# Kernel optimization log

Measured on AMD Instinct MI355X. Metric: run time of the kernel, lower is better.

Reference implementation:

```python
import jax, jax.numpy as jnp
import numpy as np

IN_F, N_ASS, OUT_F = 256, 4096, 256
P_CONNECT = 0.05
BATCH = 128


def _build_graph(in_f, n_ass, out_f, p, seed=0):
    """Replicates Random_RNN.random_graph_init edge structure (numpy, deterministic)."""
    rng = np.random.default_rng(seed)
    ass0 = in_f
    out0 = in_f + n_ass
    total = out0 + out_f
    # input -> associative edges, each input guaranteed >=1 outgoing edge
    m1 = rng.random((in_f, n_ass)) < p
    for i in np.where(~m1.any(axis=1))[0]:
        m1[i, rng.integers(n_ass)] = True
    in_src, in_dst = np.nonzero(m1)
    in_dst = in_dst + ass0
    # associative -> (associative | output) edges, each assoc >=1 outgoing edge
    m2 = rng.random((n_ass, n_ass + out_f)) < p
    for i in np.where(~m2.any(axis=1))[0]:
        m2[i, rng.integers(n_ass + out_f)] = True
    a_src, a_dst = np.nonzero(m2)
    a_src = a_src + ass0
    a_dst = a_dst + ass0
    # every output neuron guaranteed >=1 incoming edge from an associative neuron
    no_in = np.where(~m2[:, n_ass:].any(axis=0))[0]
    if no_in.size:
        a_src = np.concatenate([a_src, ass0 + rng.integers(0, n_ass, size=no_in.size)])
        a_dst = np.concatenate([a_dst, out0 + no_in])
    return (in_src.astype(np.int32), in_dst.astype(np.int32),
            a_src.astype(np.int32), a_dst.astype(np.int32), total)


def setup_inputs() -> dict:
    key = jax.random.key(0)
    k_x, k_wi, k_wa = jax.random.split(key, 3)
    in_src, in_dst, ass_src, ass_dst, total = _build_graph(IN_F, N_ASS, OUT_F, P_CONNECT)
    x = jax.random.normal(k_x, (BATCH, IN_F), dtype=jnp.float32)
    input_weights = jax.random.normal(k_wi, (in_src.shape[0],), dtype=jnp.float32) * 0.05
    associative_weights = jax.random.normal(k_wa, (ass_src.shape[0],), dtype=jnp.float32) * 0.05
    return {
        "x": x,
        "input_weights": input_weights,
        "associative_weights": associative_weights,
        "in_src": jnp.asarray(in_src),
        "in_dst": jnp.asarray(in_dst),
        "ass_src": jnp.asarray(ass_src),
        "ass_dst": jnp.asarray(ass_dst),
        "total_neurons": int(total),
        "out_features": OUT_F,
    }


def reference(x, input_weights, associative_weights, in_src, in_dst, ass_src, ass_dst,
              total_neurons, out_features):
    # Hop 1: input neurons emit x along their edges to associative neurons.
    # msg1: [E_in, B] = gather of input activations scaled by per-edge weight.
    msg1 = x.T[in_src] * input_weights[:, None]
    acc = jax.ops.segment_sum(msg1, in_dst, num_segments=total_neurons)  # [N, B]
    # Hop 2: associative neurons propagate along their edges (to assoc + output).
    msg2 = acc[ass_src] * associative_weights[:, None]  # [E_ass, B]
    acc2 = jax.ops.segment_sum(msg2, ass_dst, num_segments=total_neurons)  # [N, B]
    # Read activations of output neurons (last out_features node indices).
    return acc2[total_neurons - out_features:].T  # [B, out_features]
```

## Files before the change

kernel.cpp:

```cpp
#include <hip/hip_runtime.h>

#define IN_F   256
#define N_ASS  4096
#define OUT_F  256
#define BATCH  128
#define ASS0   256
#define OUT0   4352
#define SPLITK2 32

#define OFF_W2T (1024 * 1024)
#define OFF_P1  (2 * 1024 * 1024)
#define OFF_P2  (4 * 1024 * 1024)

__global__ __launch_bounds__(256) void zero_kernel(float4* __restrict__ w) {
    const int i = blockIdx.x * 256 + threadIdx.x;
    w[i] = make_float4(0.f, 0.f, 0.f, 0.f);
}

__global__ __launch_bounds__(256) void scatter_kernel(
        const int* __restrict__ src1, const int* __restrict__ dst1,
        const float* __restrict__ w1, int E1,
        const int* __restrict__ src2, const int* __restrict__ dst2,
        const float* __restrict__ w2, int E2,
        float* __restrict__ W1T, float* __restrict__ W2T) {
    const int e = blockIdx.x * 256 + threadIdx.x;
    if (e < E1) {
        W1T[src1[e] * N_ASS + (dst1[e] - ASS0)] = w1[e];
    } else if (e - E1 < E2) {
        const int i = e - E1;
        const int d = dst2[i];
        if (d >= OUT0)
            W2T[(src2[i] - ASS0) * OUT_F + (d - OUT0)] = w2[i];
    }
}

template<int N_, bool DUAL_A>
__global__ __launch_bounds__(256) void gemm64(const float* __restrict__ A, int lda,
                                              const float* __restrict__ B,
                                              float* __restrict__ P) {
    __shared__ __align__(16) float As[64][68];
    __shared__ __align__(16) float Bs[64][68];

    const int tid = threadIdx.x;
    const int m0 = blockIdx.x * 64;
    const int n0 = blockIdx.y * 64;
    const int z  = blockIdx.z;
    const int kBeg = z * 128;

    float4 areg[4], breg[4];
    #pragma unroll
    for (int r = 0; r < 4; ++r) {
        const int j = tid + r * 256;
        const float* ap = A + (size_t)(m0 + (j >> 4)) * lda + kBeg + (j & 15) * 4;
        areg[r] = *(const float4*)ap;
        if constexpr (DUAL_A) {
            const float4 a2 = *(const float4*)(ap + (size_t)BATCH * lda);
            areg[r].x += a2.x; areg[r].y += a2.y; areg[r].z += a2.z; areg[r].w += a2.w;
        }
        breg[r] = *(const float4*)(B + (size_t)(kBeg + (j >> 4)) * N_ + n0 + (j & 15) * 4);
    }

    const int ty4 = (tid >> 4) * 4;
    const int tx4 = (tid & 15) * 4;
    float c[4][4] = {};

    #pragma unroll
    for (int it = 0; it < 2; ++it) {
        if (it) __syncthreads();
        #pragma unroll
        for (int r = 0; r < 4; ++r) {
            const int j = tid + r * 256;
            *(float4*)&As[j >> 4][(j & 15) * 4] = areg[r];
            *(float4*)&Bs[j >> 4][(j & 15) * 4] = breg[r];
        }
        __syncthreads();
        if (it == 0) {
            const int k0 = kBeg + 64;
            #pragma unroll
            for (int r = 0; r < 4; ++r) {
                const int j = tid + r * 256;
                const float* ap = A + (size_t)(m0 + (j >> 4)) * lda + k0 + (j & 15) * 4;
                areg[r] = *(const float4*)ap;
                if constexpr (DUAL_A) {
                    const float4 a2 = *(const float4*)(ap + (size_t)BATCH * lda);
                    areg[r].x += a2.x; areg[r].y += a2.y; areg[r].z += a2.z; areg[r].w += a2.w;
                }
                breg[r] = *(const float4*)(B + (size_t)(k0 + (j >> 4)) * N_ + n0 + (j & 15) * 4);
            }
        }
        #pragma unroll
        for (int kk = 0; kk < 64; kk += 4) {
            float4 ar[4];
            #pragma unroll
            for (int i = 0; i < 4; ++i) ar[i] = *(const float4*)&As[ty4 + i][kk];
            #pragma unroll
            for (int u = 0; u < 4; ++u) {
                const float4 b = *(const float4*)&Bs[kk + u][tx4];
                #pragma unroll
                for (int i = 0; i < 4; ++i) {
                    const float a = ((const float*)&ar[i])[u];
                    c[i][0] = fmaf(a, b.x, c[i][0]);
                    c[i][1] = fmaf(a, b.y, c[i][1]);
                    c[i][2] = fmaf(a, b.z, c[i][2]);
                    c[i][3] = fmaf(a, b.w, c[i][3]);
                }
            }
        }
    }

    float* Pz = P + (size_t)z * (BATCH * N_);
    #pragma unroll
    for (int i = 0; i < 4; ++i)
        *(float4*)&Pz[(size_t)(m0 + ty4 + i) * N_ + n0 + tx4] =
            make_float4(c[i][0], c[i][1], c[i][2], c[i][3]);
}

__global__ __launch_bounds__(128) void reduce_kernel(const float4* __restrict__ P4,
                                                     float4* __restrict__ out4) {
    const int g = blockIdx.x * 128 + threadIdx.x;
    float4 s = make_float4(0.f, 0.f, 0.f, 0.f);
    #pragma unroll
    for (int z = 0; z < SPLITK2; ++z) {
        const float4 p = P4[(size_t)z * 8192 + g];
        s.x += p.x; s.y += p.y; s.z += p.z; s.w += p.w;
    }
    out4[g] = s;
}

extern "C" void kernel_launch(void* const* d_in, const int* in_sizes, int n_in,
                              void* d_out, int out_size, void* d_ws, size_t ws_size,
                              hipStream_t stream) {
    const float* x      = (const float*)d_in[0];
    const float* w_in   = (const float*)d_in[1];
    const float* w_ass  = (const float*)d_in[2];
    const int*   in_src = (const int*)d_in[3];
    const int*   in_dst = (const int*)d_in[4];
    const int*   a_src  = (const int*)d_in[5];
    const int*   a_dst  = (const int*)d_in[6];
    const int E1 = in_sizes[3];
    const int E2 = in_sizes[5];

    float* ws  = (float*)d_ws;
    float* W1T = ws;
    float* W2T = ws + OFF_W2T;
    float* P1  = ws + OFF_P1;
    float* P2  = ws + OFF_P2;
    float* out = (float*)d_out;

    zero_kernel<<<2048, 256, 0, stream>>>((float4*)d_ws);

    scatter_kernel<<<(E1 + E2 + 255) / 256, 256, 0, stream>>>(
        in_src, in_dst, w_in, E1, a_src, a_dst, w_ass, E2, W1T, W2T);

    gemm64<N_ASS, false><<<dim3(2, 64, 2), 256, 0, stream>>>(x, IN_F, W1T, P1);

    gemm64<OUT_F, true><<<dim3(2, 4, SPLITK2), 256, 0, stream>>>(P1, N_ASS, W2T, P2);

    reduce_kernel<<<64, 128, 0, stream>>>((const float4*)P2, (float4*)d_out);
}
```

Measured before the change: 40.74 us.

## Fuse zeroing and scatter into per-row dense build using sorted-source binary search

Replaces the separate workspace-zeroing kernel and the per-edge scatter kernel with one build kernel. Each block finds its source row's edge range with a cooperative binary search over the sorted src arrays, fills a zeroed shared-memory row, and writes it out with coalesced float4 stores. This removes a kernel launch and the redundant global zero pass, but it depends on the edge lists being sorted by source and adds serialized search steps with syncthreads.

After: 74.09 us. 81.9% more time.

```diff
diff --git a/kernel.cpp b/kernel.cpp
--- a/kernel.cpp
+++ b/kernel.cpp
@@ -12,25 +12,77 @@
 #define OFF_P1  (2 * 1024 * 1024)
 #define OFF_P2  (4 * 1024 * 1024)
 
-__global__ __launch_bounds__(256) void zero_kernel(float4* __restrict__ w) {
-    const int i = blockIdx.x * 256 + threadIdx.x;
-    w[i] = make_float4(0.f, 0.f, 0.f, 0.f);
-}
-
-__global__ __launch_bounds__(256) void scatter_kernel(
-        const int* __restrict__ src1, const int* __restrict__ dst1,
-        const float* __restrict__ w1, int E1,
-        const int* __restrict__ src2, const int* __restrict__ dst2,
-        const float* __restrict__ w2, int E2,
+__device__ __forceinline__ int coop_lb(const int* __restrict__ a, int n, int v,
+                                       int* __restrict__ s2) {
+    if (threadIdx.x == 0) { s2[0] = 0; s2[1] = n; }
+    __syncthreads();
+    for (;;) {
+        const int lo = s2[0], hi = s2[1];
+        const int len = hi - lo;
+        if (len <= 0) break;
+        if (len <= 256) {
+            const int idx = lo + (int)threadIdx.x;
+            const bool ge = (threadIdx.x < (unsigned)len) ? (a[idx] >= v) : true;
+            __syncthreads();
+            if (threadIdx.x == 0) s2[0] = hi;
+            __syncthreads();
+            if (threadIdx.x < (unsigned)len && ge) atomicMin(&s2[0], idx);
+            __syncthreads();
+            break;
+        }
+        const int idx = lo + 1 + (int)(((long long)threadIdx.x * (len - 2)) / 255);
+        const int av = a[idx];
+        __syncthreads();
+        if (av < v) atomicMax(&s2[0], idx + 1);
+        else        atomicMin(&s2[1], idx);
+        __syncthreads();
+    }
+    __syncthreads();
+    return s2[0];
+}
+
+__global__ __launch_bounds__(256) void build_kernel(
+        const int* __restrict__ in_src, const int* __restrict__ in_dst,
+        const float* __restrict__ w_in, int E1,
+        const int* __restrict__ a_src, const int* __restrict__ a_dst,
+        const float* __restrict__ w_ass, int E2,
         float* __restrict__ W1T, float* __restrict__ W2T) {
-    const int e = blockIdx.x * 256 + threadIdx.x;
-    if (e < E1) {
-        W1T[src1[e] * N_ASS + (dst1[e] - ASS0)] = w1[e];
-    } else if (e - E1 < E2) {
-        const int i = e - E1;
-        const int d = dst2[i];
-        if (d >= OUT0)
-            W2T[(src2[i] - ASS0) * OUT_F + (d - OUT0)] = w2[i];
+    __shared__ __align__(16) float buf[4096];
+    __shared__ int s2[2];
+    const int tid = threadIdx.x;
+    const int bid = blockIdx.x;
+
+    if (bid < 256) {
+        const int r = bid;
+        const int s = coop_lb(in_src, E1, r, s2);
+        const int e = coop_lb(in_src, E1, r + 1, s2);
+        #pragma unroll
+        for (int i = 0; i < 4; ++i)
+            *(float4*)&buf[(tid + 256 * i) * 4] = make_float4(0.f, 0.f, 0.f, 0.f);
+        __syncthreads();
+        for (int i = s + tid; i < e; i += 256)
+            buf[in_dst[i] - ASS0] = w_in[i];
+        __syncthreads();
+        float4* dst4 = (float4*)(W1T + (size_t)r * N_ASS);
+        #pragma unroll
+        for (int i = 0; i < 4; ++i) dst4[tid + 256 * i] = ((const float4*)buf)[tid + 256 * i];
+    } else {
+        const int r0 = (bid - 256) * 8;
+        const int s = coop_lb(a_src, E2, ASS0 + r0, s2);
+        const int e = coop_lb(a_src, E2, ASS0 + r0 + 8, s2);
+        #pragma unroll
+        for (int i = 0; i < 2; ++i)
+            *(float4*)&buf[(tid + 256 * i) * 4] = make_float4(0.f, 0.f, 0.f, 0.f);
+        __syncthreads();
+        for (int i = s + tid; i < e; i += 256) {
+            const int d = a_dst[i];
+            if (d >= OUT0)
+                buf[(a_src[i] - ASS0 - r0) * OUT_F + (d - OUT0)] = w_ass[i];
+        }
+        __syncthreads();
+        float4* dst4 = (float4*)(W2T + (size_t)r0 * OUT_F);
+        #pragma unroll
+        for (int i = 0; i < 2; ++i) dst4[tid + 256 * i] = ((const float4*)buf)[tid + 256 * i];
     }
 }
 
@@ -145,12 +197,9 @@
     float* W2T = ws + OFF_W2T;
     float* P1  = ws + OFF_P1;
     float* P2  = ws + OFF_P2;
-    float* out = (float*)d_out;
-
-    zero_kernel<<<2048, 256, 0, stream>>>((float4*)d_ws);
-
-    scatter_kernel<<<(E1 + E2 + 255) / 256, 256, 0, stream>>>(
-        in_src, in_dst, w_in, E1, a_src, a_dst, w_ass, E2, W1T, W2T);
+
+    build_kernel<<<768, 256, 0, stream>>>(in_src, in_dst, w_in, E1,
+                                          a_src, a_dst, w_ass, E2, W1T, W2T);
 
     gemm64<N_ASS, false><<<dim3(2, 64, 2), 256, 0, stream>>>(x, IN_F, W1T, P1);
 
```

## Fuse both GEMM hops into one kernel keeping intermediate slice in LDS

Applied to the files above, without the earlier changes.

Replaces the two split-K GEMM launches with a single fused kernel. Each block computes x·W1T for a 64-wide slice of associative neurons, keeps that intermediate tile in shared memory, and immediately multiplies it by the matching 64-row slice of W2T. Per-slice partial outputs are written and summed by the reduce kernel over 64 slices. This removes the intermediate P1 round trip through global memory and one launch, at the cost of more partials to reduce (64 vs 32) and a large LDS footprint that lowers occupancy. W2 uses an XOR-swizzled shared layout to limit bank conflicts.

Result: slower. 58.78 us (+44.3%).

```diff
diff --git a/kernel.cpp b/kernel.cpp
--- a/kernel.cpp
+++ b/kernel.cpp
@@ -6,11 +6,11 @@
 #define BATCH  128
 #define ASS0   256
 #define OUT0   4352
-#define SPLITK2 32
+#define NSLICE 64
+#define MROWS  32
 
 #define OFF_W2T (1024 * 1024)
-#define OFF_P1  (2 * 1024 * 1024)
-#define OFF_P2  (4 * 1024 * 1024)
+#define OFF_P   (2 * 1024 * 1024)
 
 __global__ __launch_bounds__(256) void zero_kernel(float4* __restrict__ w) {
     const int i = blockIdx.x * 256 + threadIdx.x;
@@ -34,85 +34,117 @@
     }
 }
 
-template<int N_, bool DUAL_A>
-__global__ __launch_bounds__(256) void gemm64(const float* __restrict__ A, int lda,
-                                              const float* __restrict__ B,
-                                              float* __restrict__ P) {
-    __shared__ __align__(16) float As[64][68];
-    __shared__ __align__(16) float Bs[64][68];
+__global__ __launch_bounds__(256) void fused_gemm(
+        const float* __restrict__ x,
+        const float* __restrict__ W1T,
+        const float* __restrict__ W2T,
+        float* __restrict__ P) {
+    __shared__ __align__(16) float Xs[MROWS][260];
+    __shared__ __align__(16) float W1s[64][68];
+    __shared__ __align__(16) float Tls[MROWS][68];
+    __shared__ __align__(16) float W2s[64][256];
 
     const int tid = threadIdx.x;
-    const int m0 = blockIdx.x * 64;
-    const int n0 = blockIdx.y * 64;
-    const int z  = blockIdx.z;
-    const int kBeg = z * 128;
+    const int m0 = blockIdx.x * MROWS;
+    const int s0 = blockIdx.y * 64;
 
-    float4 areg[4], breg[4];
-    #pragma unroll
-    for (int r = 0; r < 4; ++r) {
-        const int j = tid + r * 256;
-        const float* ap = A + (size_t)(m0 + (j >> 4)) * lda + kBeg + (j & 15) * 4;
-        areg[r] = *(const float4*)ap;
-        if constexpr (DUAL_A) {
-            const float4 a2 = *(const float4*)(ap + (size_t)BATCH * lda);
-            areg[r].x += a2.x; areg[r].y += a2.y; areg[r].z += a2.z; areg[r].w += a2.w;
+    {
+        const float4* src = (const float4*)(x + (size_t)m0 * IN_F);
+        #pragma unroll
+        for (int i = 0; i < 8; ++i) {
+            const int f = tid + i * 256;
+            *(float4*)&Xs[f >> 6][(f & 63) * 4] = src[f];
         }
-        breg[r] = *(const float4*)(B + (size_t)(kBeg + (j >> 4)) * N_ + n0 + (j & 15) * 4);
     }
 
-    const int ty4 = (tid >> 4) * 4;
-    const int tx4 = (tid & 15) * 4;
-    float c[4][4] = {};
+    const int ty = (tid >> 4) * 2;
+    const int tx = (tid & 15) * 4;
+    const int wrow = tid >> 4;
+    const int wj   = tid & 15;
+    float ta[2][4] = {};
 
-    #pragma unroll
-    for (int it = 0; it < 2; ++it) {
-        if (it) __syncthreads();
+    for (int kp = 0; kp < 4; ++kp) {
+        float4 w2r[4];
         #pragma unroll
-        for (int r = 0; r < 4; ++r) {
-            const int j = tid + r * 256;
-            *(float4*)&As[j >> 4][(j & 15) * 4] = areg[r];
-            *(float4*)&Bs[j >> 4][(j & 15) * 4] = breg[r];
+        for (int i = 0; i < 4; ++i) {
+            const int j = wj + 16 * i;
+            w2r[i] = *(const float4*)(W2T + (size_t)(s0 + kp * 16 + wrow) * OUT_F + j * 4);
+        }
+        float4 w1v[4];
+        #pragma unroll
+        for (int i = 0; i < 4; ++i) {
+            const int r = (tid >> 4) + 16 * i;
+            w1v[i] = *(const float4*)(W1T + (size_t)(kp * 64 + r) * N_ASS + s0 + wj * 4);
         }
         __syncthreads();
-        if (it == 0) {
-            const int k0 = kBeg + 64;
-            #pragma unroll
-            for (int r = 0; r < 4; ++r) {
-                const int j = tid + r * 256;
-                const float* ap = A + (size_t)(m0 + (j >> 4)) * lda + k0 + (j & 15) * 4;
-                areg[r] = *(const float4*)ap;
-                if constexpr (DUAL_A) {
-                    const float4 a2 = *(const float4*)(ap + (size_t)BATCH * lda);
-                    areg[r].x += a2.x; areg[r].y += a2.y; areg[r].z += a2.z; areg[r].w += a2.w;
-                }
-                breg[r] = *(const float4*)(B + (size_t)(k0 + (j >> 4)) * N_ + n0 + (j & 15) * 4);
-            }
+        #pragma unroll
+        for (int i = 0; i < 4; ++i)
+            *(float4*)&W1s[(tid >> 4) + 16 * i][wj * 4] = w1v[i];
+        #pragma unroll
+        for (int i = 0; i < 4; ++i) {
+            const int j = wj + 16 * i;
+            const int sj = j ^ ((j >> 3) & 7);
+            *(float4*)&W2s[kp * 16 + wrow][sj * 4] = w2r[i];
         }
+        __syncthreads();
         #pragma unroll
-        for (int kk = 0; kk < 64; kk += 4) {
-            float4 ar[4];
-            #pragma unroll
-            for (int i = 0; i < 4; ++i) ar[i] = *(const float4*)&As[ty4 + i][kk];
+        for (int k = 0; k < 64; k += 4) {
+            const float4 a0 = *(const float4*)&Xs[ty][kp * 64 + k];
+            const float4 a1 = *(const float4*)&Xs[ty + 1][kp * 64 + k];
             #pragma unroll
             for (int u = 0; u < 4; ++u) {
-                const float4 b = *(const float4*)&Bs[kk + u][tx4];
-                #pragma unroll
-                for (int i = 0; i < 4; ++i) {
-                    const float a = ((const float*)&ar[i])[u];
-                    c[i][0] = fmaf(a, b.x, c[i][0]);
-                    c[i][1] = fmaf(a, b.y, c[i][1]);
-                    c[i][2] = fmaf(a, b.z, c[i][2]);
-                    c[i][3] = fmaf(a, b.w, c[i][3]);
-                }
+                const float4 b = *(const float4*)&W1s[k + u][tx];
+                const float a0u = ((const float*)&a0)[u];
+                const float a1u = ((const float*)&a1)[u];
+                ta[0][0] = fmaf(a0u, b.x, ta[0][0]); ta[0][1] = fmaf(a0u, b.y, ta[0][1]);
+                ta[0][2] = fmaf(a0u, b.z, ta[0][2]); ta[0][3] = fmaf(a0u, b.w, ta[0][3]);
+                ta[1][0] = fmaf(a1u, b.x, ta[1][0]); ta[1][1] = fmaf(a1u, b.y, ta[1][1]);
+                ta[1][2] = fmaf(a1u, b.z, ta[1][2]); ta[1][3] = fmaf(a1u, b.w, ta[1][3]);
             }
         }
     }
+    *(float4*)&Tls[ty][tx]     = make_float4(ta[0][0], ta[0][1], ta[0][2], ta[0][3]);
+    *(float4*)&Tls[ty + 1][tx] = make_float4(ta[1][0], ta[1][1], ta[1][2], ta[1][3]);
+    __syncthreads();
 
-    float* Pz = P + (size_t)z * (BATCH * N_);
+    const int o0 = (tid & 15) * 16;
+    const float* wp[4];
     #pragma unroll
-    for (int i = 0; i < 4; ++i)
-        *(float4*)&Pz[(size_t)(m0 + ty4 + i) * N_ + n0 + tx4] =
-            make_float4(c[i][0], c[i][1], c[i][2], c[i][3]);
+    for (int j = 0; j < 4; ++j) {
+        const int f = (o0 >> 2) + j;
+        const int sf = f ^ ((f >> 3) & 7);
+        wp[j] = &W2s[0][0] + sf * 4;
+    }
+    float pa[2][16] = {};
+    #pragma unroll
+    for (int k4 = 0; k4 < 64; k4 += 4) {
+        const float4 t0 = *(const float4*)&Tls[ty][k4];
+        const float4 t1 = *(const float4*)&Tls[ty + 1][k4];
+        #pragma unroll
+        for (int u = 0; u < 4; ++u) {
+            const float tv0 = ((const float*)&t0)[u];
+            const float tv1 = ((const float*)&t1)[u];
+            #pragma unroll
+            for (int j = 0; j < 4; ++j) {
+                const float4 w = *(const float4*)(wp[j] + (k4 + u) * 256);
+                pa[0][j*4+0] = fmaf(tv0, w.x, pa[0][j*4+0]);
+                pa[0][j*4+1] = fmaf(tv0, w.y, pa[0][j*4+1]);
+                pa[0][j*4+2] = fmaf(tv0, w.z, pa[0][j*4+2]);
+                pa[0][j*4+3] = fmaf(tv0, w.w, pa[0][j*4+3]);
+                pa[1][j*4+0] = fmaf(tv1, w.x, pa[1][j*4+0]);
+                pa[1][j*4+1] = fmaf(tv1, w.y, pa[1][j*4+1]);
+                pa[1][j*4+2] = fmaf(tv1, w.z, pa[1][j*4+2]);
+                pa[1][j*4+3] = fmaf(tv1, w.w, pa[1][j*4+3]);
+            }
+        }
+    }
+    float* Pb = P + (size_t)blockIdx.y * (BATCH * OUT_F) + (size_t)m0 * OUT_F;
+    #pragma unroll
+    for (int i = 0; i < 2; ++i)
+        #pragma unroll
+        for (int j = 0; j < 4; ++j)
+            *(float4*)&Pb[(size_t)(ty + i) * OUT_F + o0 + j * 4] =
+                make_float4(pa[i][j*4+0], pa[i][j*4+1], pa[i][j*4+2], pa[i][j*4+3]);
 }
 
 __global__ __launch_bounds__(128) void reduce_kernel(const float4* __restrict__ P4,
@@ -120,7 +152,7 @@
     const int g = blockIdx.x * 128 + threadIdx.x;
     float4 s = make_float4(0.f, 0.f, 0.f, 0.f);
     #pragma unroll
-    for (int z = 0; z < SPLITK2; ++z) {
+    for (int z = 0; z < NSLICE; ++z) {
         const float4 p = P4[(size_t)z * 8192 + g];
         s.x += p.x; s.y += p.y; s.z += p.z; s.w += p.w;
     }
@@ -143,18 +175,14 @@
     float* ws  = (float*)d_ws;
     float* W1T = ws;
     float* W2T = ws + OFF_W2T;
-    float* P1  = ws + OFF_P1;
-    float* P2  = ws + OFF_P2;
-    float* out = (float*)d_out;
+    float* P   = ws + OFF_P;
 
     zero_kernel<<<2048, 256, 0, stream>>>((float4*)d_ws);
 
     scatter_kernel<<<(E1 + E2 + 255) / 256, 256, 0, stream>>>(
         in_src, in_dst, w_in, E1, a_src, a_dst, w_ass, E2, W1T, W2T);
 
-    gemm64<N_ASS, false><<<dim3(2, 64, 2), 256, 0, stream>>>(x, IN_F, W1T, P1);
+    fused_gemm<<<dim3(4, NSLICE), 256, 0, stream>>>(x, W1T, W2T, P);
 
-    gemm64<OUT_F, true><<<dim3(2, 4, SPLITK2), 256, 0, stream>>>(P1, N_ASS, W2T, P2);
-
-    reduce_kernel<<<64, 128, 0, stream>>>((const float4*)P2, (float4*)d_out);
+    reduce_kernel<<<64, 128, 0, stream>>>((const float4*)P, (float4*)d_out);
 }
```
